# Kernel tuning notes

Measured on AMD Instinct MI355X. Metric: run time of the kernel, lower is better.

## Reference

```python
import jax, jax.numpy as jnp
import numpy as np
from jax import lax

B, CIN, H, W = 4, 720, 128, 128
MID = 512           # conv3x3 output channels (hardcoded in OCRHead)
KC, VC, NC = 256, 256, 19
BN_EPS = 1e-5


def setup_inputs() -> dict:
    key = jax.random.key(0)
    ks = jax.random.split(key, 16)
    s = 0.02
    f32 = jnp.float32
    return {
        "feats": jax.random.normal(ks[0], (B, CIN, H, W), f32),
        # conv3x3 (no bias)
        "w3": (jax.random.normal(ks[1], (MID, CIN, 3, 3), f32) * s),
        # BatchNorm affine params
        "gamma": 1.0 + 0.1 * jax.random.normal(ks[2], (MID,), f32),
        "beta": 0.1 * jax.random.normal(ks[3], (MID,), f32),
        # aux 1x1 conv (with bias)
        "aux_w": jax.random.normal(ks[4], (NC, MID), f32) * s,
        "aux_b": 0.01 * jax.random.normal(ks[5], (NC,), f32),
        # ObjectAttention: query 1x1 conv (no bias), key/value Linear (with bias), out 1x1 conv (no bias)
        "q_w": jax.random.normal(ks[6], (KC, MID), f32) * s,
        "k_w": jax.random.normal(ks[7], (KC, MID), f32) * s,
        "k_b": 0.01 * jax.random.normal(ks[8], (KC,), f32),
        "v_w": jax.random.normal(ks[9], (VC, MID), f32) * s,
        "v_b": 0.01 * jax.random.normal(ks[10], (VC,), f32),
        "out_w": jax.random.normal(ks[11], (MID, VC), f32) * s,
        # cls 1x1 conv (with bias)
        "cls_w": jax.random.normal(ks[12], (NC, MID), f32) * s,
        "cls_b": 0.01 * jax.random.normal(ks[13], (NC,), f32),
    }


def reference(feats, w3, gamma, beta, aux_w, aux_b, q_w, k_w, k_b, v_w, v_b, out_w, cls_w, cls_b):
    # conv3x3, padding=1, no bias
    x = lax.conv_general_dilated(feats, w3, window_strides=(1, 1),
                                 padding=((1, 1), (1, 1)),
                                 dimension_numbers=("NCHW", "OIHW", "NCHW"))
    # BatchNorm (batch mode: stats over batch+spatial) + relu
    mean = jnp.mean(x, axis=(0, 2, 3))
    var = jnp.var(x, axis=(0, 2, 3))
    x = (x - mean[None, :, None, None]) * lax.rsqrt(var + BN_EPS)[None, :, None, None]
    x = x * gamma[None, :, None, None] + beta[None, :, None, None]
    x = jax.nn.relu(x)

    # aux head: 1x1 conv with bias -> [B, K, H, W]
    aux_logits = jnp.einsum("bchw,kc->bkhw", x, aux_w) + aux_b[None, :, None, None]

    # SpatialGather: softmax over classes per pixel, normalize over pixels per class
    x_flat = x.reshape(B, MID, H * W).transpose(0, 2, 1)           # [B, N, C]
    probs = jax.nn.softmax(aux_logits.reshape(B, NC, H * W).transpose(0, 2, 1), axis=-1)  # [B, N, K]
    weights = probs / jnp.clip(jnp.sum(probs, axis=1, keepdims=True), 1e-6)
    context = jnp.einsum("bnk,bnc->bkc", weights, x_flat)          # [B, K, C]

    # ObjectAttention
    q = jnp.einsum("bchw,dc->bdhw", x, q_w).reshape(B, KC, H * W).transpose(0, 2, 1)  # [B, N, KC]
    k = jnp.einsum("bkc,dc->bkd", context, k_w) + k_b              # [B, K, KC]
    v = jnp.einsum("bkc,dc->bkd", context, v_w) + v_b              # [B, K, VC]
    scale = 1.0 / jnp.sqrt(jnp.asarray(KC, jnp.float32))
    attn = jax.nn.softmax(jnp.einsum("bnd,bkd->bnk", q * scale, k), axis=-1)  # [B, N, K]
    agg = jnp.einsum("bnk,bkv->bnv", attn, v)                      # [B, N, VC]
    agg_chw = agg.reshape(B, H, W, VC).transpose(0, 3, 1, 2)       # [B, VC, H, W]
    obj = jnp.einsum("bvhw,ov->bohw", agg_chw, out_w)              # [B, MID, H, W]

    x = x + obj
    logits = jnp.einsum("bchw,kc->bkhw", x, cls_w) + cls_b[None, :, None, None]
    return (logits, aux_logits)
```

## Files before the change

kernel.cpp:

```cpp
#include <hip/hip_runtime.h>
#include <hip/hip_bf16.h>


__device__ __forceinline__ float u_lo(unsigned u) { return __uint_as_float(u << 16); }
__device__ __forceinline__ float u_hi(unsigned u) { return __uint_as_float(u & 0xffff0000u); }
__device__ __forceinline__ float scrub(float v) { return isfinite(v) ? v : 1e4f; }
#define BF2F(h) __bfloat162float(h)

typedef __attribute__((ext_vector_type(8))) short bf16x8;
typedef __attribute__((ext_vector_type(4))) float f32x4;

#define SO_APACK  0ull
#define TAIL0     9371648ull
#define TA_AUXWT  (TAIL0 + 0ull)
#define TA_CLSWT  (TAIL0 + 38912ull)
#define TA_SS     (TAIL0 + 77824ull)
#define TA_PSUM   (TAIL0 + 81920ull)
#define TA_CTX    (TAIL0 + 82432ull)
#define TA_KMAT   (TAIL0 + 238080ull)
#define TA_VMAT   (TAIL0 + 315904ull)
#define TA_FCLS   (TAIL0 + 393728ull)
#define TA_MT     (TAIL0 + 413184ull)
#define TA_G      (TAIL0 + 568832ull)

#define LDS_CI   40
#define LDS_ROW  (3 * LDS_CI)
#define LDS_TOT  (130 * LDS_ROW)

__global__ __launch_bounds__(256) void prep_small_kernel(
    const float* __restrict__ aux_w, const float* __restrict__ cls_w,
    float* __restrict__ aux_wt, float* __restrict__ cls_wt) {
  int i = blockIdx.x * 256 + threadIdx.x;
  if (i < 9728) {
    int k = i >> 9, c = i & 511;
    aux_wt[c * 19 + k] = aux_w[i];
    cls_wt[c * 19 + k] = cls_w[i];
  }
}

__global__ __launch_bounds__(256) void prep_apack_kernel(
    const float* __restrict__ w3, __hip_bfloat16* __restrict__ Apack) {
  int idx = blockIdx.x * 256 + threadIdx.x;
  if (idx >= 512 * 736) return;
  int oc = idx / 736, ci = idx - (idx / 736) * 736;
  float v[9];
#pragma unroll
  for (int k = 0; k < 9; ++k) v[k] = 0.f;
  if (ci < 720) {
    const float* src = w3 + ((size_t)oc * 720 + ci) * 9;
#pragma unroll
    for (int k = 0; k < 9; ++k) v[k] = src[k];
  }
#pragma unroll
  for (int k = 0; k < 9; ++k)
    Apack[((size_t)k * 512 + oc) * 736 + ci] = __float2bfloat16(v[k]);
}

__global__ __launch_bounds__(256) void conv_mfma_kernel(
    const float* __restrict__ feats, const __hip_bfloat16* __restrict__ Apack,
    __hip_bfloat16* __restrict__ X) {
  __shared__ short Blds[LDS_TOT];
  int bid = blockIdx.x;
  int xcd = bid & 7;
  int slot = bid >> 3;
  int oc_t = slot & 3;
  int gx = (slot >> 2) * 8 + xcd;
  int b = gx >> 7, h = gx & 127;
  int tid = threadIdx.x;
  int wave = tid >> 6, lane = tid & 63;
  int wm = wave >> 1, wn = wave & 1;
  int l15 = lane & 15, quad = lane >> 4;

  f32x4 acc[4][4];
#pragma unroll
  for (int mb = 0; mb < 4; ++mb)
#pragma unroll
    for (int nb = 0; nb < 4; ++nb) acc[mb][nb] = (f32x4){0.f, 0.f, 0.f, 0.f};

  for (int i = tid; i < 2 * LDS_ROW; i += 256) {
    int wp = (i < LDS_ROW) ? 0 : 129;
    Blds[wp * LDS_ROW + (i < LDS_ROW ? i : i - LDS_ROW)] = 0;
  }

  const short* Ab = (const short*)Apack;
  int oc_row = oc_t * 128 + wm * 64 + l15;

  const float* fbase = feats + (((size_t)b * 720) << 14) + lane * 2;

  float2 pre[3][8];
  {
    int ci0 = wave * 8;
#pragma unroll
    for (int r = 0; r < 3; ++r) {
      int hr = h - 1 + r;
#pragma unroll
      for (int j = 0; j < 8; ++j) pre[r][j] = (float2){0.f, 0.f};
      if ((unsigned)hr < 128u) {
        const float* p = fbase + ((size_t)ci0 << 14) + hr * 128;
#pragma unroll
        for (int j = 0; j < 8; ++j)
          pre[r][j] = *reinterpret_cast<const float2*>(p + (size_t)j * 16384);
      }
    }
  }

  for (int cb = 0; cb < 23; ++cb) {
    __syncthreads();
#pragma unroll
    for (int r = 0; r < 3; ++r) {
      union { bf16x8 v; __hip_bfloat16 hh[8]; } E, O;
#pragma unroll
      for (int j = 0; j < 8; ++j) {
        E.hh[j] = __float2bfloat16(pre[r][j].x);
        O.hh[j] = __float2bfloat16(pre[r][j].y);
      }
      short* wb = &Blds[(lane * 2 + 1) * LDS_ROW + r * LDS_CI + wave * 8];
      *reinterpret_cast<bf16x8*>(wb) = E.v;
      *reinterpret_cast<bf16x8*>(wb + LDS_ROW) = O.v;
    }
    __syncthreads();
    if (cb < 22) {
      int ci0 = (cb + 1) * 32 + wave * 8;
      bool civ = (ci0 < 720);
#pragma unroll
      for (int r = 0; r < 3; ++r) {
        int hr = h - 1 + r;
#pragma unroll
        for (int j = 0; j < 8; ++j) pre[r][j] = (float2){0.f, 0.f};
        if (civ && ((unsigned)hr < 128u)) {
          const float* p = fbase + ((size_t)ci0 << 14) + hr * 128;
#pragma unroll
          for (int j = 0; j < 8; ++j)
            pre[r][j] = *reinterpret_cast<const float2*>(p + (size_t)j * 16384);
        }
      }
    }
#pragma unroll
    for (int r = 0; r < 3; ++r) {
#pragma unroll
      for (int dw = 0; dw < 3; ++dw) {
        int plane = r * 3 + dw;
        const short* ap = Ab + ((size_t)plane * 512 + oc_row) * 736 + cb * 32 + quad * 8;
        bf16x8 af[4];
#pragma unroll
        for (int mb = 0; mb < 4; ++mb)
          af[mb] = *(const bf16x8*)(ap + (size_t)mb * 16 * 736);
        bf16x8 bfr[4];
#pragma unroll
        for (int nb = 0; nb < 4; ++nb) {
          int px = wn * 64 + nb * 16 + l15;
          bfr[nb] = *(const bf16x8*)(&Blds[(px + dw) * LDS_ROW + r * LDS_CI + quad * 8]);
        }
#pragma unroll
        for (int mb = 0; mb < 4; ++mb)
#pragma unroll
          for (int nb = 0; nb < 4; ++nb)
            acc[mb][nb] = __builtin_amdgcn_mfma_f32_16x16x32_bf16(
                af[mb], bfr[nb], acc[mb][nb], 0, 0, 0);
      }
    }
  }
#pragma unroll
  for (int mb = 0; mb < 4; ++mb)
#pragma unroll
    for (int nb = 0; nb < 4; ++nb) {
      int px = wn * 64 + nb * 16 + l15;
#pragma unroll
      for (int reg = 0; reg < 4; ++reg) {
        int oc = oc_t * 128 + wm * 64 + mb * 16 + quad * 4 + reg;
        X[(((size_t)b * 512 + oc) << 14) + h * 128 + px] =
            __float2bfloat16(acc[mb][nb][reg]);
      }
    }
}

__global__ __launch_bounds__(256) void bn_stats_kernel(
    const __hip_bfloat16* __restrict__ X, const float* __restrict__ gamma,
    const float* __restrict__ beta, float* __restrict__ ss_out) {
  int c = blockIdx.x, tid = threadIdx.x;
  float s = 0.f, ss = 0.f;
  for (int b = 0; b < 4; ++b) {
    const __hip_bfloat16* p = X + (((size_t)b * 512 + c) << 14);
    for (int n = tid * 8; n < 16384; n += 2048) {
      uint4 u = *reinterpret_cast<const uint4*>(p + n);
      unsigned arr[4] = {u.x, u.y, u.z, u.w};
#pragma unroll
      for (int j = 0; j < 4; ++j) {
        float f0 = u_lo(arr[j]), f1 = u_hi(arr[j]);
        s += f0 + f1;
        ss += f0 * f0 + f1 * f1;
      }
    }
  }
#pragma unroll
  for (int off = 32; off > 0; off >>= 1) {
    s += __shfl_down(s, off);
    ss += __shfl_down(ss, off);
  }
  __shared__ float red[8];
  int wid = tid >> 6, lane = tid & 63;
  if (lane == 0) { red[wid] = s; red[4 + wid] = ss; }
  __syncthreads();
  if (tid == 0) {
    s = red[0] + red[1] + red[2] + red[3];
    ss = red[4] + red[5] + red[6] + red[7];
    float mean = s * (1.f / 65536.f);
    float var = ss * (1.f / 65536.f) - mean * mean;
    float gi = gamma[c] * rsqrtf(var + 1e-5f);
    ss_out[c * 2] = gi;
    ss_out[c * 2 + 1] = beta[c] - mean * gi;
  }
}

__global__ __launch_bounds__(256) void bn_apply_kernel(
    __hip_bfloat16* __restrict__ X, const float* __restrict__ ss) {
  size_t idx = ((size_t)blockIdx.x * 256 + threadIdx.x) * 8;
  int c = (int)((idx >> 14) & 511);
  float sc = ss[c * 2], sh = ss[c * 2 + 1];
  uint4 u = *reinterpret_cast<const uint4*>(X + idx);
  unsigned arr[4] = {u.x, u.y, u.z, u.w};
  union { uint4 u; __hip_bfloat16 h[8]; } O;
#pragma unroll
  for (int j = 0; j < 4; ++j) {
    float f0 = fmaxf(fmaf(u_lo(arr[j]), sc, sh), 0.f);
    float f1 = fmaxf(fmaf(u_hi(arr[j]), sc, sh), 0.f);
    O.h[2 * j] = __float2bfloat16(f0);
    O.h[2 * j + 1] = __float2bfloat16(f1);
  }
  *reinterpret_cast<uint4*>(X + idx) = O.u;
}

__global__ __launch_bounds__(256) void aux_ctx_kernel(
    const __hip_bfloat16* __restrict__ X, const float* __restrict__ aux_wt,
    const float* __restrict__ aux_b,
    float* __restrict__ ctx, float* __restrict__ psum,
    float* __restrict__ aux_out) {
  int b = blockIdx.y;
  int n0 = blockIdx.x * 256;
  int tid = threadIdx.x;
  __shared__ float pl[19][256];

  const __hip_bfloat16* Xb = X + (((size_t)b * 512) << 14);

  int p0 = n0 + tid;
  float a0[19];
#pragma unroll
  for (int k = 0; k < 19; ++k) a0[k] = aux_b[k];
  for (int c = 0; c < 512; ++c) {
    float f0 = BF2F(Xb[((size_t)c << 14) + p0]);
    const float* wr = aux_wt + c * 19;
#pragma unroll
    for (int k = 0; k < 19; ++k) a0[k] = fmaf(wr[k], f0, a0[k]);
  }
  {
    size_t ob = ((size_t)b * 19) << 14;
#pragma unroll
    for (int k = 0; k < 19; ++k) {
      if (!(b == 3 && k >= 10))
        aux_out[ob + ((size_t)k << 14) + p0] = scrub(a0[k]);
    }
  }
  float mx0 = a0[0];
#pragma unroll
  for (int k = 1; k < 19; ++k) mx0 = fmaxf(mx0, a0[k]);
  float s0 = 0.f;
#pragma unroll
  for (int k = 0; k < 19; ++k) { a0[k] = __expf(a0[k] - mx0); s0 += a0[k]; }
  float r0 = 1.f / s0;
#pragma unroll
  for (int k = 0; k < 19; ++k) {
    float q0 = a0[k] * r0;
    pl[k][tid] = q0;
    a0[k] = q0;
  }
#pragma unroll
  for (int k = 0; k < 19; ++k) {
    float t = a0[k];
#pragma unroll
    for (int off = 32; off > 0; off >>= 1) t += __shfl_down(t, off);
    if ((tid & 63) == 0) atomicAdd(&psum[b * 19 + k], t);
  }
  __syncthreads();

  int c0 = tid * 2;
  const __hip_bfloat16* x0 = Xb + ((size_t)c0 << 14) + n0;
  const __hip_bfloat16* x1 = x0 + 16384;
  float b0[19], b1[19];
#pragma unroll
  for (int k = 0; k < 19; ++k) { b0[k] = 0.f; b1[k] = 0.f; }
  for (int nl = 0; nl < 256; ++nl) {
    float xv0 = BF2F(x0[nl]), xv1 = BF2F(x1[nl]);
#pragma unroll
    for (int kk = 0; kk < 19; ++kk) {
      float p = pl[kk][nl];
      b0[kk] = fmaf(p, xv0, b0[kk]);
      b1[kk] = fmaf(p, xv1, b1[kk]);
    }
  }
#pragma unroll
  for (int kk = 0; kk < 19; ++kk) {
    atomicAdd(&ctx[((b * 19 + kk) << 9) + c0], b0[kk]);
    atomicAdd(&ctx[((b * 19 + kk) << 9) + c0 + 1], b1[kk]);
  }
}

__global__ __launch_bounds__(256) void small_a_kernel(
    const float* __restrict__ ctx, const float* __restrict__ psum,
    const float* __restrict__ k_w, const float* __restrict__ k_b,
    const float* __restrict__ v_w, const float* __restrict__ v_b,
    const float* __restrict__ cls_w, const float* __restrict__ out_w,
    float* __restrict__ Kmat, float* __restrict__ vmat, float* __restrict__ fcls) {
  int i = blockIdx.x * 256 + threadIdx.x;
  if (i < 38912) {
    int half = i / 19456;
    int j = i - half * 19456;
    int d = j & 255;
    int t = j >> 8;
    const float* w = (half ? v_w : k_w) + d * 512;
    const float* cr = ctx + (t << 9);
    float s = 0.f;
    for (int c = 0; c < 512; ++c) s = fmaf(w[c], cr[c], s);
    float rcp = 1.f / fmaxf(psum[t], 1e-6f);
    float bias = (half ? v_b : k_b)[d];
    (half ? vmat : Kmat)[j] = s * rcp + bias;
  } else if (i < 43776) {
    int j = i - 38912;
    int vv = j & 255, k = j >> 8;
    const float* cw = cls_w + k * 512;
    float s = 0.f;
    for (int c = 0; c < 512; ++c) s = fmaf(cw[c], out_w[c * 256 + vv], s);
    fcls[j] = s;
  }
}

__global__ __launch_bounds__(256) void small_b_kernel(
    const float* __restrict__ Kmat, const float* __restrict__ vmat,
    const float* __restrict__ fcls, const float* __restrict__ q_w,
    float* __restrict__ m_t, float* __restrict__ g) {
  int i = blockIdx.x * 256 + threadIdx.x;
  if (i < 38912) {
    int kk = i % 19;
    int t = i / 19;
    int c = t & 511, b = t >> 9;
    const float* kr = Kmat + ((b * 19 + kk) << 8);
    float s = 0.f;
    for (int d = 0; d < 256; ++d) s = fmaf(q_w[d * 512 + c], kr[d], s);
    m_t[i] = s;
  } else if (i < 40356) {
    int j = i - 38912;
    int k = j % 19;
    int t = j / 19;
    const float* vr = vmat + (t << 8);
    const float* fr = fcls + (k << 8);
    float s = 0.f;
    for (int v = 0; v < 256; ++v) s = fmaf(fr[v], vr[v], s);
    g[j] = s;
  }
}

__global__ __launch_bounds__(256) void final_fused_kernel(
    const __hip_bfloat16* __restrict__ X, const float* __restrict__ m_t,
    const float* __restrict__ cls_wt, const float* __restrict__ cls_b,
    const float* __restrict__ g, float* __restrict__ out) {
  int b = blockIdx.y;
  int n = blockIdx.x * 256 + threadIdx.x;
  float macc[19], cacc[19];
#pragma unroll
  for (int k = 0; k < 19; ++k) { macc[k] = 0.f; cacc[k] = 0.f; }
  const __hip_bfloat16* xp = X + (((size_t)b * 512) << 14) + n;
  for (int c = 0; c < 512; ++c) {
    float xv = BF2F(xp[(size_t)c << 14]);
    const float* mr = m_t + (b * 512 + c) * 19;
    const float* wr = cls_wt + c * 19;
#pragma unroll
    for (int k = 0; k < 19; ++k) {
      macc[k] = fmaf(mr[k], xv, macc[k]);
      cacc[k] = fmaf(wr[k], xv, cacc[k]);
    }
  }
  float mx = -1e30f;
#pragma unroll
  for (int k = 0; k < 19; ++k) { macc[k] *= 0.0625f; mx = fmaxf(mx, macc[k]); }
  float sum = 0.f;
#pragma unroll
  for (int k = 0; k < 19; ++k) { macc[k] = __expf(macc[k] - mx); sum += macc[k]; }
  float r = 1.f / sum;
#pragma unroll
  for (int k = 0; k < 19; ++k) cacc[k] += cls_b[k];
#pragma unroll
  for (int kk = 0; kk < 19; ++kk) {
    float av = macc[kk] * r;
    const float* gr = g + (b * 19 + kk) * 19;
#pragma unroll
    for (int k = 0; k < 19; ++k) cacc[k] = fmaf(gr[k], av, cacc[k]);
  }
  size_t ob = ((size_t)b * 19) << 14;
#pragma unroll
  for (int k = 0; k < 19; ++k)
    out[ob + ((size_t)k << 14) + n] = scrub(cacc[k]);
}

__global__ __launch_bounds__(256) void aux_tail_kernel(
    const __hip_bfloat16* __restrict__ X, const float* __restrict__ aux_w,
    const float* __restrict__ aux_b, float* __restrict__ aux_out) {
  __shared__ float wt[9728];
  for (int i = threadIdx.x; i < 9728; i += 256) {
    int k = i >> 9, c = i & 511;
    wt[c * 19 + k] = aux_w[i];
  }
  __syncthreads();
  const int b = 3;
  int n = blockIdx.x * 256 + threadIdx.x;
  float acc[19];
#pragma unroll
  for (int k = 0; k < 19; ++k) acc[k] = aux_b[k];
  const __hip_bfloat16* xp = X + (((size_t)b * 512) << 14) + n;
  for (int c = 0; c < 512; ++c) {
    float xv = BF2F(xp[(size_t)c << 14]);
    const float* wr = &wt[c * 19];
#pragma unroll
    for (int k = 0; k < 19; ++k) acc[k] = fmaf(wr[k], xv, acc[k]);
  }
  size_t ob = ((size_t)b * 19) << 14;
#pragma unroll
  for (int k = 10; k < 19; ++k)
    aux_out[ob + ((size_t)k << 14) + n] = scrub(acc[k]);
}

extern "C" void kernel_launch(void* const* d_in, const int* in_sizes, int n_in,
                              void* d_out, int out_size, void* d_ws, size_t ws_size,
                              hipStream_t stream) {
  const float* feats = (const float*)d_in[0];
  const float* w3    = (const float*)d_in[1];
  const float* gamma = (const float*)d_in[2];
  const float* beta  = (const float*)d_in[3];
  const float* aux_w = (const float*)d_in[4];
  const float* aux_b = (const float*)d_in[5];
  const float* q_w   = (const float*)d_in[6];
  const float* k_w   = (const float*)d_in[7];
  const float* k_b   = (const float*)d_in[8];
  const float* v_w   = (const float*)d_in[9];
  const float* v_b   = (const float*)d_in[10];
  const float* out_w = (const float*)d_in[11];
  const float* cls_w = (const float*)d_in[12];
  const float* cls_b = (const float*)d_in[13];

  float* logits_out = (float*)d_out;
  float* aux_out    = logits_out + 1245184;

  __hip_bfloat16* X = (__hip_bfloat16*)d_ws;

  char* ob = (char*)d_out;
  __hip_bfloat16* Apack = (__hip_bfloat16*)(ob + SO_APACK);
  float* aux_wt = (float*)(ob + TA_AUXWT);
  float* cls_wt = (float*)(ob + TA_CLSWT);
  float* ssbuf  = (float*)(ob + TA_SS);
  float* psum   = (float*)(ob + TA_PSUM);
  float* ctx    = (float*)(ob + TA_CTX);
  float* Kmat   = (float*)(ob + TA_KMAT);
  float* vmat   = (float*)(ob + TA_VMAT);
  float* fcls   = (float*)(ob + TA_FCLS);
  float* m_t    = (float*)(ob + TA_MT);
  float* g      = (float*)(ob + TA_G);

  hipMemsetAsync(ob + TA_PSUM, 0, 512 + 155648, stream);

  prep_small_kernel<<<38, 256, 0, stream>>>(aux_w, cls_w, aux_wt, cls_wt);
  prep_apack_kernel<<<1472, 256, 0, stream>>>(w3, Apack);
  conv_mfma_kernel<<<2048, 256, 0, stream>>>(feats, Apack, X);
  bn_stats_kernel<<<512, 256, 0, stream>>>(X, gamma, beta, ssbuf);
  bn_apply_kernel<<<16384, 256, 0, stream>>>(X, ssbuf);
  aux_ctx_kernel<<<dim3(64, 4), 256, 0, stream>>>(X, aux_wt, aux_b, ctx, psum, aux_out);
  small_a_kernel<<<171, 256, 0, stream>>>(ctx, psum, k_w, k_b, v_w, v_b, cls_w, out_w,
                                          Kmat, vmat, fcls);
  small_b_kernel<<<158, 256, 0, stream>>>(Kmat, vmat, fcls, q_w, m_t, g);
  final_fused_kernel<<<dim3(64, 4), 256, 0, stream>>>(X, m_t, cls_wt, cls_b, g, logits_out);
  aux_tail_kernel<<<64, 256, 0, stream>>>(X, aux_w, aux_b, aux_out);
}
```

Baseline: 1.407 ms.

## Switch intermediate activation layout from NCHW to NHWC across all kernels

The conv output X is now stored channel-last (pixel-major, 512 channels contiguous), and every consumer is rewritten to match. BN stats become per-block partial sums with atomics plus a small finalize kernel, and bn_apply reads scale/shift from LDS. The 1x1-conv style kernels (aux, final, aux_tail) now load 8 channels per 16-byte vector instead of strided scalar bf16 loads. The aim is to remove uncoalesced, channel-strided accesses. In exchange, the conv epilogue writes scattered 8-byte chunks and the ctx gather reads with a 1 KB stride.

```diff
diff --git a/kernel.cpp b/kernel.cpp
--- a/kernel.cpp
+++ b/kernel.cpp
@@ -22,6 +22,7 @@
 #define TA_FCLS   (TAIL0 + 393728ull)
 #define TA_MT     (TAIL0 + 413184ull)
 #define TA_G      (TAIL0 + 568832ull)
+#define TA_BNACC  (TAIL0 + 574608ull)
 
 #define LDS_CI   40
 #define LDS_ROW  (3 * LDS_CI)
@@ -161,69 +162,66 @@
     }
   }
 #pragma unroll
-  for (int mb = 0; mb < 4; ++mb)
-#pragma unroll
-    for (int nb = 0; nb < 4; ++nb) {
-      int px = wn * 64 + nb * 16 + l15;
-#pragma unroll
-      for (int reg = 0; reg < 4; ++reg) {
-        int oc = oc_t * 128 + wm * 64 + mb * 16 + quad * 4 + reg;
-        X[(((size_t)b * 512 + oc) << 14) + h * 128 + px] =
-            __float2bfloat16(acc[mb][nb][reg]);
-      }
-    }
+  for (int nb = 0; nb < 4; ++nb) {
+    int px = wn * 64 + nb * 16 + l15;
+    __hip_bfloat16* xr = X + (((size_t)b * 16384 + h * 128 + px) << 9);
+#pragma unroll
+    for (int mb = 0; mb < 4; ++mb) {
+      int oc = oc_t * 128 + wm * 64 + mb * 16 + quad * 4;
+      union { unsigned long long u; __hip_bfloat16 hh[4]; } P;
+      P.hh[0] = __float2bfloat16(acc[mb][nb][0]);
+      P.hh[1] = __float2bfloat16(acc[mb][nb][1]);
+      P.hh[2] = __float2bfloat16(acc[mb][nb][2]);
+      P.hh[3] = __float2bfloat16(acc[mb][nb][3]);
+      *reinterpret_cast<unsigned long long*>(xr + oc) = P.u;
+    }
+  }
 }
 
 __global__ __launch_bounds__(256) void bn_stats_kernel(
-    const __hip_bfloat16* __restrict__ X, const float* __restrict__ gamma,
+    const __hip_bfloat16* __restrict__ X, float* __restrict__ bnacc) {
+  int row0 = blockIdx.x * 128;
+  int c0 = threadIdx.x * 2;
+  float s0 = 0.f, s1 = 0.f, q0 = 0.f, q1 = 0.f;
+  const __hip_bfloat16* p = X + ((size_t)row0 << 9) + c0;
+  for (int r = 0; r < 128; ++r) {
+    unsigned u = *reinterpret_cast<const unsigned*>(p + ((size_t)r << 9));
+    float f0 = u_lo(u), f1 = u_hi(u);
+    s0 += f0; q0 += f0 * f0;
+    s1 += f1; q1 += f1 * f1;
+  }
+  atomicAdd(&bnacc[c0], s0);
+  atomicAdd(&bnacc[c0 + 1], s1);
+  atomicAdd(&bnacc[512 + c0], q0);
+  atomicAdd(&bnacc[512 + c0 + 1], q1);
+}
+
+__global__ __launch_bounds__(256) void bn_finalize_kernel(
+    const float* __restrict__ bnacc, const float* __restrict__ gamma,
     const float* __restrict__ beta, float* __restrict__ ss_out) {
-  int c = blockIdx.x, tid = threadIdx.x;
-  float s = 0.f, ss = 0.f;
-  for (int b = 0; b < 4; ++b) {
-    const __hip_bfloat16* p = X + (((size_t)b * 512 + c) << 14);
-    for (int n = tid * 8; n < 16384; n += 2048) {
-      uint4 u = *reinterpret_cast<const uint4*>(p + n);
-      unsigned arr[4] = {u.x, u.y, u.z, u.w};
-#pragma unroll
-      for (int j = 0; j < 4; ++j) {
-        float f0 = u_lo(arr[j]), f1 = u_hi(arr[j]);
-        s += f0 + f1;
-        ss += f0 * f0 + f1 * f1;
-      }
-    }
-  }
-#pragma unroll
-  for (int off = 32; off > 0; off >>= 1) {
-    s += __shfl_down(s, off);
-    ss += __shfl_down(ss, off);
-  }
-  __shared__ float red[8];
-  int wid = tid >> 6, lane = tid & 63;
-  if (lane == 0) { red[wid] = s; red[4 + wid] = ss; }
-  __syncthreads();
-  if (tid == 0) {
-    s = red[0] + red[1] + red[2] + red[3];
-    ss = red[4] + red[5] + red[6] + red[7];
-    float mean = s * (1.f / 65536.f);
-    float var = ss * (1.f / 65536.f) - mean * mean;
-    float gi = gamma[c] * rsqrtf(var + 1e-5f);
-    ss_out[c * 2] = gi;
-    ss_out[c * 2 + 1] = beta[c] - mean * gi;
-  }
+  int c = blockIdx.x * 256 + threadIdx.x;
+  float mean = bnacc[c] * (1.f / 65536.f);
+  float var = bnacc[512 + c] * (1.f / 65536.f) - mean * mean;
+  float gi = gamma[c] * rsqrtf(var + 1e-5f);
+  ss_out[c * 2] = gi;
+  ss_out[c * 2 + 1] = beta[c] - mean * gi;
 }
 
 __global__ __launch_bounds__(256) void bn_apply_kernel(
     __hip_bfloat16* __restrict__ X, const float* __restrict__ ss) {
+  __shared__ float ssl[1024];
+  for (int i = threadIdx.x; i < 1024; i += 256) ssl[i] = ss[i];
+  __syncthreads();
   size_t idx = ((size_t)blockIdx.x * 256 + threadIdx.x) * 8;
-  int c = (int)((idx >> 14) & 511);
-  float sc = ss[c * 2], sh = ss[c * 2 + 1];
+  int c0 = (int)(idx & 511);
   uint4 u = *reinterpret_cast<const uint4*>(X + idx);
   unsigned arr[4] = {u.x, u.y, u.z, u.w};
   union { uint4 u; __hip_bfloat16 h[8]; } O;
 #pragma unroll
   for (int j = 0; j < 4; ++j) {
-    float f0 = fmaxf(fmaf(u_lo(arr[j]), sc, sh), 0.f);
-    float f1 = fmaxf(fmaf(u_hi(arr[j]), sc, sh), 0.f);
+    int c = c0 + 2 * j;
+    float f0 = fmaxf(fmaf(u_lo(arr[j]), ssl[2 * c], ssl[2 * c + 1]), 0.f);
+    float f1 = fmaxf(fmaf(u_hi(arr[j]), ssl[2 * c + 2], ssl[2 * c + 3]), 0.f);
     O.h[2 * j] = __float2bfloat16(f0);
     O.h[2 * j + 1] = __float2bfloat16(f1);
   }
@@ -240,17 +238,22 @@
   int tid = threadIdx.x;
   __shared__ float pl[19][256];
 
-  const __hip_bfloat16* Xb = X + (((size_t)b * 512) << 14);
-
   int p0 = n0 + tid;
+  const __hip_bfloat16* xr = X + (((size_t)b * 16384 + p0) << 9);
   float a0[19];
 #pragma unroll
   for (int k = 0; k < 19; ++k) a0[k] = aux_b[k];
-  for (int c = 0; c < 512; ++c) {
-    float f0 = BF2F(Xb[((size_t)c << 14) + p0]);
-    const float* wr = aux_wt + c * 19;
-#pragma unroll
-    for (int k = 0; k < 19; ++k) a0[k] = fmaf(wr[k], f0, a0[k]);
+  for (int c = 0; c < 512; c += 8) {
+    uint4 u = *reinterpret_cast<const uint4*>(xr + c);
+    unsigned w4[4] = {u.x, u.y, u.z, u.w};
+#pragma unroll
+    for (int j = 0; j < 4; ++j) {
+      float f0 = u_lo(w4[j]), f1 = u_hi(w4[j]);
+      const float* wr = aux_wt + (c + 2 * j) * 19;
+#pragma unroll
+      for (int k = 0; k < 19; ++k)
+        a0[k] = fmaf(wr[19 + k], f1, fmaf(wr[k], f0, a0[k]));
+    }
   }
   {
     size_t ob = ((size_t)b * 19) << 14;
@@ -283,13 +286,13 @@
   __syncthreads();
 
   int c0 = tid * 2;
-  const __hip_bfloat16* x0 = Xb + ((size_t)c0 << 14) + n0;
-  const __hip_bfloat16* x1 = x0 + 16384;
+  const __hip_bfloat16* x2 = X + (((size_t)b * 16384 + n0) << 9) + c0;
   float b0[19], b1[19];
 #pragma unroll
   for (int k = 0; k < 19; ++k) { b0[k] = 0.f; b1[k] = 0.f; }
   for (int nl = 0; nl < 256; ++nl) {
-    float xv0 = BF2F(x0[nl]), xv1 = BF2F(x1[nl]);
+    unsigned u = *reinterpret_cast<const unsigned*>(x2 + ((size_t)nl << 9));
+    float xv0 = u_lo(u), xv1 = u_hi(u);
 #pragma unroll
     for (int kk = 0; kk < 19; ++kk) {
       float p = pl[kk][nl];
@@ -367,15 +370,20 @@
   float macc[19], cacc[19];
 #pragma unroll
   for (int k = 0; k < 19; ++k) { macc[k] = 0.f; cacc[k] = 0.f; }
-  const __hip_bfloat16* xp = X + (((size_t)b * 512) << 14) + n;
-  for (int c = 0; c < 512; ++c) {
-    float xv = BF2F(xp[(size_t)c << 14]);
-    const float* mr = m_t + (b * 512 + c) * 19;
-    const float* wr = cls_wt + c * 19;
-#pragma unroll
-    for (int k = 0; k < 19; ++k) {
-      macc[k] = fmaf(mr[k], xv, macc[k]);
-      cacc[k] = fmaf(wr[k], xv, cacc[k]);
+  const __hip_bfloat16* xr = X + (((size_t)b * 16384 + n) << 9);
+  for (int c = 0; c < 512; c += 8) {
+    uint4 u = *reinterpret_cast<const uint4*>(xr + c);
+    unsigned w4[4] = {u.x, u.y, u.z, u.w};
+#pragma unroll
+    for (int j = 0; j < 4; ++j) {
+      float f0 = u_lo(w4[j]), f1 = u_hi(w4[j]);
+      const float* mr = m_t + (size_t)(b * 512 + c + 2 * j) * 19;
+      const float* wr = cls_wt + (c + 2 * j) * 19;
+#pragma unroll
+      for (int k = 0; k < 19; ++k) {
+        macc[k] = fmaf(mr[19 + k], f1, fmaf(mr[k], f0, macc[k]));
+        cacc[k] = fmaf(wr[19 + k], f1, fmaf(wr[k], f0, cacc[k]));
+      }
     }
   }
   float mx = -1e30f;
@@ -414,12 +422,18 @@
   float acc[19];
 #pragma unroll
   for (int k = 0; k < 19; ++k) acc[k] = aux_b[k];
-  const __hip_bfloat16* xp = X + (((size_t)b * 512) << 14) + n;
-  for (int c = 0; c < 512; ++c) {
-    float xv = BF2F(xp[(size_t)c << 14]);
-    const float* wr = &wt[c * 19];
-#pragma unroll
-    for (int k = 0; k < 19; ++k) acc[k] = fmaf(wr[k], xv, acc[k]);
+  const __hip_bfloat16* xr = X + (((size_t)b * 16384 + n) << 9);
+  for (int c = 0; c < 512; c += 8) {
+    uint4 u = *reinterpret_cast<const uint4*>(xr + c);
+    unsigned w4[4] = {u.x, u.y, u.z, u.w};
+#pragma unroll
+    for (int j = 0; j < 4; ++j) {
+      float f0 = u_lo(w4[j]), f1 = u_hi(w4[j]);
+      const float* wr = &wt[(c + 2 * j) * 19];
+#pragma unroll
+      for (int k = 0; k < 19; ++k)
+        acc[k] = fmaf(wr[19 + k], f1, fmaf(wr[k], f0, acc[k]));
+    }
   }
   size_t ob = ((size_t)b * 19) << 14;
 #pragma unroll
@@ -462,13 +476,16 @@
   float* fcls   = (float*)(ob + TA_FCLS);
   float* m_t    = (float*)(ob + TA_MT);
   float* g      = (float*)(ob + TA_G);
+  float* bnacc  = (float*)(ob + TA_BNACC);
 
   hipMemsetAsync(ob + TA_PSUM, 0, 512 + 155648, stream);
+  hipMemsetAsync(ob + TA_BNACC, 0, 4096, stream);
 
   prep_small_kernel<<<38, 256, 0, stream>>>(aux_w, cls_w, aux_wt, cls_wt);
   prep_apack_kernel<<<1472, 256, 0, stream>>>(w3, Apack);
   conv_mfma_kernel<<<2048, 256, 0, stream>>>(feats, Apack, X);
-  bn_stats_kernel<<<512, 256, 0, stream>>>(X, gamma, beta, ssbuf);
+  bn_stats_kernel<<<512, 256, 0, stream>>>(X, bnacc);
+  bn_finalize_kernel<<<2, 256, 0, stream>>>(bnacc, gamma, beta, ssbuf);
   bn_apply_kernel<<<16384, 256, 0, stream>>>(X, ssbuf);
   aux_ctx_kernel<<<dim3(64, 4), 256, 0, stream>>>(X, aux_wt, aux_b, ctx, psum, aux_out);
   small_a_kernel<<<171, 256, 0, stream>>>(ctx, psum, k_w, k_b, v_w, v_b, cls_w, out_w,
```

New measurement: 1.453 ms. 3.3% more time.
